# Optimization experiments

Measured on AMD Instinct MI355X. Metric: run time of the kernel, lower is better.

The kernel has to match this reference:

```python
import jax, jax.numpy as jnp
import numpy as np

IN_FEATURES = 4096
OUT_FEATURES = 4096
OUTLIER_NUM = 128
Q_IN = IN_FEATURES - OUTLIER_NUM  # 3968
B, S = 4, 2048


def _build_perm(seed=0):
    rng = np.random.default_rng(seed)
    outlier_ids = rng.choice(IN_FEATURES, size=OUTLIER_NUM, replace=False)
    mask = np.ones(IN_FEATURES, dtype=bool)
    mask[outlier_ids] = False
    col_ids = np.arange(IN_FEATURES, dtype=np.int32)
    col_perm = np.concatenate([col_ids[mask], col_ids[~mask]])
    inv_col_perm = np.zeros(IN_FEATURES, dtype=np.int32)
    inv_col_perm[col_perm] = np.arange(IN_FEATURES, dtype=np.int32)
    return inv_col_perm


def setup_inputs() -> dict:
    key = jax.random.key(0)
    k1, k2, k3, k4, k5 = jax.random.split(key, 5)
    inp = {
        "input": jax.random.normal(k1, (B, S, IN_FEATURES), dtype=jnp.float32),
        # low-bit integer codes stored as float (e.g. int4 range), per-row scale
        "q_weight": jax.random.randint(k2, (OUT_FEATURES, Q_IN), -8, 8).astype(jnp.float32),
        "fp_weight": jax.random.normal(k3, (OUT_FEATURES, OUTLIER_NUM), dtype=jnp.float32),
        "alpha_scale": jax.random.uniform(k4, (OUT_FEATURES, 1), dtype=jnp.float32, minval=0.01, maxval=0.1),
        "bias": jax.random.normal(k5, (OUT_FEATURES,), dtype=jnp.float32),
        "inv_col_perm": jnp.asarray(_build_perm(), dtype=jnp.int32),
    }
    return inp


def reference(input, q_weight, fp_weight, alpha_scale, bias, inv_col_perm):
    # SymQuant.dequantize: per-output-row symmetric scale
    dq_w = q_weight * alpha_scale                      # [O, Q_IN]
    out_w = jnp.concatenate([dq_w, fp_weight], axis=1)  # [O, IN]
    out_w = out_w[:, inv_col_perm]                      # undo column permutation
    # F.linear: input @ out_w.T + bias
    return jnp.einsum("bsi,oi->bso", input, out_w) + bias
```

## Files before the change

### kernel.cpp

```cpp
#include <hip/hip_runtime.h>
#include <stdint.h>

#define IN_F  4096
#define OUT_F 4096
#define OUTL  128
#define QIN   (IN_F - OUTL)
#define MTOT  8192
#define BM 128
#define BN 128
#define BKB 128

typedef unsigned short u16;
typedef int i32x4 __attribute__((ext_vector_type(4)));

__global__ __launch_bounds__(256) void prep_fused(
    const float* __restrict__ A, signed char* __restrict__ A8,
    float* __restrict__ s_arr,
    const float* __restrict__ qw, const float* __restrict__ fpw,
    const float* __restrict__ alpha, const int* __restrict__ invp,
    signed char* __restrict__ W8, float* __restrict__ t_arr) {
  const int tid = threadIdx.x;
  __shared__ float red[4];

  if (blockIdx.x >= OUT_F) {
    const int m = blockIdx.x - OUT_F;
    const float* row = A + (size_t)m * IN_F;
    float4 v[4];
    float amax = 0.f;
#pragma unroll
    for (int k = 0; k < 4; ++k) {
      v[k] = ((const float4*)row)[k * 256 + tid];
      amax = fmaxf(amax, fmaxf(fmaxf(fabsf(v[k].x), fabsf(v[k].y)),
                               fmaxf(fabsf(v[k].z), fabsf(v[k].w))));
    }
#pragma unroll
    for (int off = 32; off; off >>= 1)
      amax = fmaxf(amax, __shfl_xor(amax, off, 64));
    if ((tid & 63) == 0) red[tid >> 6] = amax;
    __syncthreads();
    amax = fmaxf(fmaxf(red[0], red[1]), fmaxf(red[2], red[3]));
    const float inv = 127.f / amax;
    if (tid == 0) s_arr[m] = amax / 127.f;
#pragma unroll
    for (int k = 0; k < 4; ++k) {
      const int q0 = __float2int_rn(v[k].x * inv);
      const int q1 = __float2int_rn(v[k].y * inv);
      const int q2 = __float2int_rn(v[k].z * inv);
      const int q3 = __float2int_rn(v[k].w * inv);
      const uint32_t p = (q0 & 255) | ((q1 & 255) << 8) |
                         ((q2 & 255) << 16) | ((uint32_t)(q3 & 255) << 24);
      ((uint32_t*)A8)[(size_t)m * (IN_F / 4) + k * 256 + tid] = p;
    }
  } else {
    const int o = blockIdx.x;
    __shared__ float qs[QIN];
    __shared__ float fs[OUTL];
    const float a = alpha[o];
    float amax = 0.f;
    const float4* qrow = (const float4*)(qw + (size_t)o * QIN);
#pragma unroll
    for (int k = 0; k < 4; ++k) {
      const int idx = k * 256 + tid;
      if (idx < QIN / 4) {
        const float4 q = qrow[idx];
        ((float4*)qs)[idx] = q;
        const float qm = fmaxf(fmaxf(fabsf(q.x), fabsf(q.y)),
                               fmaxf(fabsf(q.z), fabsf(q.w)));
        amax = fmaxf(amax, qm * a);
      }
    }
    if (tid < OUTL / 4) {
      const float4 f = ((const float4*)(fpw + (size_t)o * OUTL))[tid];
      ((float4*)fs)[tid] = f;
      amax = fmaxf(amax, fmaxf(fmaxf(fabsf(f.x), fabsf(f.y)),
                               fmaxf(fabsf(f.z), fabsf(f.w))));
    }
#pragma unroll
    for (int off = 32; off; off >>= 1)
      amax = fmaxf(amax, __shfl_xor(amax, off, 64));
    if ((tid & 63) == 0) red[tid >> 6] = amax;
    __syncthreads();
    amax = fmaxf(fmaxf(red[0], red[1]), fmaxf(red[2], red[3]));
    const float invws = 127.f / amax;
    if (tid == 0) t_arr[o] = amax / 127.f;

    signed char vals[16];
#pragma unroll
    for (int q = 0; q < 4; ++q) {
      const int4 jj = ((const int4*)invp)[tid * 4 + q];
      const int j[4] = {jj.x, jj.y, jj.z, jj.w};
#pragma unroll
      for (int e = 0; e < 4; ++e) {
        const float v = (j[e] < QIN) ? qs[j[e]] * a : fs[j[e] - QIN];
        vals[q * 4 + e] = (signed char)__float2int_rn(v * invws);
      }
    }
    ((uint4*)(W8 + (size_t)o * IN_F))[tid] = *(const uint4*)vals;
  }
}

#define GLDS(g, l)                                                              \
  __builtin_amdgcn_global_load_lds(                                             \
      (const __attribute__((address_space(1))) void*)(g),                       \
      (__attribute__((address_space(3))) void*)(l), 16, 0, 0)

__global__ __launch_bounds__(256, 3) void gemm_i8(
    const signed char* __restrict__ A8, const signed char* __restrict__ W8,
    const float* __restrict__ s_arr, const float* __restrict__ t_arr,
    const float* __restrict__ bias, float* __restrict__ C) {
  __shared__ unsigned char As8[BM * BKB];
  __shared__ unsigned char Bs8[BN * BKB];

  const int tid  = threadIdx.x;
  const int wave = tid >> 6;
  const int lane = tid & 63;
  const int bn = blockIdx.x, bm = blockIdx.y;
  const int wm = (wave >> 1) * 64;
  const int wn = (wave & 1)  * 64;

  const int srow   = wave * 32 + (lane >> 3);
  const int schunk = (lane & 7) ^ ((lane >> 3) & 7);
  const signed char* Ag = A8 + (size_t)(bm * BM + srow) * IN_F + schunk * 16;
  const signed char* Wg = W8 + (size_t)(bn * BN + srow) * IN_F + schunk * 16;
  unsigned char* AsW = As8 + wave * 32 * BKB;
  unsigned char* BsW = Bs8 + wave * 32 * BKB;

  i32x4 acc[4][4];
#pragma unroll
  for (int mi = 0; mi < 4; ++mi)
#pragma unroll
    for (int ni = 0; ni < 4; ++ni) acc[mi][ni] = (i32x4){0, 0, 0, 0};

  const int fr = lane & 15;
  const int fq = lane >> 4;

  for (int kt = 0; kt < IN_F / BKB; ++kt) {
    __syncthreads();
#pragma unroll
    for (int t = 0; t < 4; ++t) {
      GLDS(Ag + kt * BKB + t * 8 * IN_F, AsW + t * 8 * BKB);
      GLDS(Wg + kt * BKB + t * 8 * IN_F, BsW + t * 8 * BKB);
    }
    __syncthreads();

#pragma unroll
    for (int ks = 0; ks < 2; ++ks) {
      i32x4 af[4], bg[4];
#pragma unroll
      for (int mi = 0; mi < 4; ++mi)
        af[mi] = *(const i32x4*)
            &As8[(wm + mi * 16 + fr) * BKB + (((ks * 4 + fq) ^ (fr & 7)) * 16)];
#pragma unroll
      for (int ni = 0; ni < 4; ++ni)
        bg[ni] = *(const i32x4*)
            &Bs8[(wn + ni * 16 + fr) * BKB + (((ks * 4 + fq) ^ (fr & 7)) * 16)];
#pragma unroll
      for (int mi = 0; mi < 4; ++mi)
#pragma unroll
        for (int ni = 0; ni < 4; ++ni)
          acc[mi][ni] = __builtin_amdgcn_mfma_i32_16x16x64_i8(
              af[mi], bg[ni], acc[mi][ni], 0, 0, 0);
    }
  }

  float sv[4][4];
#pragma unroll
  for (int mi = 0; mi < 4; ++mi)
#pragma unroll
    for (int rr = 0; rr < 4; ++rr)
      sv[mi][rr] = s_arr[bm * BM + wm + mi * 16 + fq * 4 + rr];

#pragma unroll
  for (int ni = 0; ni < 4; ++ni) {
    const int n = bn * BN + wn + ni * 16 + fr;
    const float tn = t_arr[n];
    const float bv = bias[n];
#pragma unroll
    for (int mi = 0; mi < 4; ++mi) {
      const int m0 = bm * BM + wm + mi * 16 + fq * 4;
#pragma unroll
      for (int rr = 0; rr < 4; ++rr)
        C[(size_t)(m0 + rr) * OUT_F + n] =
            (float)acc[mi][ni][rr] * (sv[mi][rr] * tn) + bv;
    }
  }
}

extern "C" void kernel_launch(void* const* d_in, const int* in_sizes, int n_in,
                              void* d_out, int out_size, void* d_ws, size_t ws_size,
                              hipStream_t stream) {
  const float* input = (const float*)d_in[0];
  const float* qw    = (const float*)d_in[1];
  const float* fpw   = (const float*)d_in[2];
  const float* alpha = (const float*)d_in[3];
  const float* bias  = (const float*)d_in[4];
  const int*   invp  = (const int*)d_in[5];

  char* ws = (char*)d_ws;
  signed char* A8    = (signed char*)ws;
  signed char* W8    = (signed char*)(ws + (32ull << 20));
  float* s_arr = (float*)(ws + (48ull << 20));
  float* t_arr = (float*)(ws + (48ull << 20) + (64ull << 10));
  float* out = (float*)d_out;

  prep_fused<<<OUT_F + MTOT, 256, 0, stream>>>(input, A8, s_arr, qw, fpw,
                                               alpha, invp, W8, t_arr);

  dim3 ggrid(OUT_F / BN, MTOT / BM);
  gemm_i8<<<ggrid, dim3(256), 0, stream>>>(A8, W8, s_arr, t_arr, bias, out);
}
```

Measured before the change: 409.9 us.

## Double-buffer int8 GEMM with 256x256 tiles, 512 threads and swizzled block order

Grows the GEMM tile from 128x128 to 256x256 with 8 waves, each holding a 128x64 accumulator. K tiles are double-buffered so the next tile's global-to-LDS loads overlap the current tile's MFMAs, and a remapped 1D grid groups blocks for better cache locality. MFMA sections get raised wave priority. The prep kernel also pads its shared staging array to reduce LDS bank conflicts in the permuted gather. The cost is higher register and LDS pressure and only 512 blocks in the grid.

```diff
diff --git a/kernel.cpp b/kernel.cpp
--- a/kernel.cpp
+++ b/kernel.cpp
@@ -6,9 +6,10 @@
 #define OUTL  128
 #define QIN   (IN_F - OUTL)
 #define MTOT  8192
-#define BM 128
-#define BN 128
+#define BM 256
+#define BN 256
 #define BKB 128
+#define NKT (IN_F / BKB)
 
 typedef unsigned short u16;
 typedef int i32x4 __attribute__((ext_vector_type(4)));
@@ -53,7 +54,7 @@
     }
   } else {
     const int o = blockIdx.x;
-    __shared__ float qs[QIN];
+    __shared__ float qs[QIN + (QIN >> 4)];
     __shared__ float fs[OUTL];
     const float a = alpha[o];
     float amax = 0.f;
@@ -63,7 +64,11 @@
       const int idx = k * 256 + tid;
       if (idx < QIN / 4) {
         const float4 q = qrow[idx];
-        ((float4*)qs)[idx] = q;
+        const int b0 = idx * 4 + (idx >> 2);
+        qs[b0]     = q.x;
+        qs[b0 + 1] = q.y;
+        qs[b0 + 2] = q.z;
+        qs[b0 + 3] = q.w;
         const float qm = fmaxf(fmaxf(fabsf(q.x), fabsf(q.y)),
                                fmaxf(fabsf(q.z), fabsf(q.w)));
         amax = fmaxf(amax, qm * a);
@@ -91,7 +96,8 @@
       const int j[4] = {jj.x, jj.y, jj.z, jj.w};
 #pragma unroll
       for (int e = 0; e < 4; ++e) {
-        const float v = (j[e] < QIN) ? qs[j[e]] * a : fs[j[e] - QIN];
+        const int je = j[e];
+        const float v = (je < QIN) ? qs[je + (je >> 4)] * a : fs[je - QIN];
         vals[q * 4 + e] = (signed char)__float2int_rn(v * invws);
       }
     }
@@ -104,68 +110,93 @@
       (const __attribute__((address_space(1))) void*)(g),                       \
       (__attribute__((address_space(3))) void*)(l), 16, 0, 0)
 
-__global__ __launch_bounds__(256, 3) void gemm_i8(
+__global__ __launch_bounds__(512, 2) void gemm_i8(
     const signed char* __restrict__ A8, const signed char* __restrict__ W8,
     const float* __restrict__ s_arr, const float* __restrict__ t_arr,
     const float* __restrict__ bias, float* __restrict__ C) {
-  __shared__ unsigned char As8[BM * BKB];
-  __shared__ unsigned char Bs8[BN * BKB];
+  __shared__ unsigned char As8[2][BM * BKB];
+  __shared__ unsigned char Bs8[2][BN * BKB];
 
   const int tid  = threadIdx.x;
   const int wave = tid >> 6;
   const int lane = tid & 63;
-  const int bn = blockIdx.x, bm = blockIdx.y;
-  const int wm = (wave >> 1) * 64;
-  const int wn = (wave & 1)  * 64;
+
+  const int bid = ((blockIdx.x & 7) << 6) | ((int)blockIdx.x >> 3);
+  const int bm = bid >> 4;
+  const int bn = bid & 15;
+
+  const int wm = (wave >> 2) * 128;
+  const int wn = (wave & 3) * 64;
 
   const int srow   = wave * 32 + (lane >> 3);
   const int schunk = (lane & 7) ^ ((lane >> 3) & 7);
   const signed char* Ag = A8 + (size_t)(bm * BM + srow) * IN_F + schunk * 16;
   const signed char* Wg = W8 + (size_t)(bn * BN + srow) * IN_F + schunk * 16;
-  unsigned char* AsW = As8 + wave * 32 * BKB;
-  unsigned char* BsW = Bs8 + wave * 32 * BKB;
-
-  i32x4 acc[4][4];
-#pragma unroll
-  for (int mi = 0; mi < 4; ++mi)
+  const int sdst = wave * 32 * BKB;
+
+  i32x4 acc[8][4];
+#pragma unroll
+  for (int mi = 0; mi < 8; ++mi)
 #pragma unroll
     for (int ni = 0; ni < 4; ++ni) acc[mi][ni] = (i32x4){0, 0, 0, 0};
 
   const int fr = lane & 15;
   const int fq = lane >> 4;
 
-  for (int kt = 0; kt < IN_F / BKB; ++kt) {
-    __syncthreads();
+  int aoff[8], boff[4], ck[2];
+  ck[0] = ((0 + fq) ^ (fr & 7)) * 16;
+  ck[1] = ((4 + fq) ^ (fr & 7)) * 16;
+#pragma unroll
+  for (int mi = 0; mi < 8; ++mi) aoff[mi] = (wm + mi * 16 + fr) * BKB;
+#pragma unroll
+  for (int ni = 0; ni < 4; ++ni) boff[ni] = (wn + ni * 16 + fr) * BKB;
+
+  auto STAGE = [&](int buf, int kt) {
 #pragma unroll
     for (int t = 0; t < 4; ++t) {
-      GLDS(Ag + kt * BKB + t * 8 * IN_F, AsW + t * 8 * BKB);
-      GLDS(Wg + kt * BKB + t * 8 * IN_F, BsW + t * 8 * BKB);
-    }
-    __syncthreads();
-
+      GLDS(Ag + (size_t)kt * BKB + t * 8 * IN_F, &As8[buf][sdst + t * 8 * BKB]);
+      GLDS(Wg + (size_t)kt * BKB + t * 8 * IN_F, &Bs8[buf][sdst + t * 8 * BKB]);
+    }
+  };
+
+  auto COMPUTE = [&](int buf) {
 #pragma unroll
     for (int ks = 0; ks < 2; ++ks) {
-      i32x4 af[4], bg[4];
-#pragma unroll
-      for (int mi = 0; mi < 4; ++mi)
-        af[mi] = *(const i32x4*)
-            &As8[(wm + mi * 16 + fr) * BKB + (((ks * 4 + fq) ^ (fr & 7)) * 16)];
+      i32x4 bg[4], af[8];
 #pragma unroll
       for (int ni = 0; ni < 4; ++ni)
-        bg[ni] = *(const i32x4*)
-            &Bs8[(wn + ni * 16 + fr) * BKB + (((ks * 4 + fq) ^ (fr & 7)) * 16)];
-#pragma unroll
-      for (int mi = 0; mi < 4; ++mi)
+        bg[ni] = *(const i32x4*)&Bs8[buf][boff[ni] + ck[ks]];
+#pragma unroll
+      for (int mi = 0; mi < 8; ++mi)
+        af[mi] = *(const i32x4*)&As8[buf][aoff[mi] + ck[ks]];
+      __builtin_amdgcn_s_setprio(1);
+#pragma unroll
+      for (int mi = 0; mi < 8; ++mi)
 #pragma unroll
         for (int ni = 0; ni < 4; ++ni)
           acc[mi][ni] = __builtin_amdgcn_mfma_i32_16x16x64_i8(
               af[mi], bg[ni], acc[mi][ni], 0, 0, 0);
-    }
+      __builtin_amdgcn_s_setprio(0);
+    }
+  };
+
+  STAGE(0, 0);
+
+  for (int kt = 0; kt < NKT - 1; ++kt) {
+    STAGE((kt & 1) ^ 1, kt + 1);
+    asm volatile("s_waitcnt vmcnt(8)" ::: "memory");
+    __builtin_amdgcn_s_barrier();
+    COMPUTE(kt & 1);
+    asm volatile("s_waitcnt lgkmcnt(0)" ::: "memory");
+    __builtin_amdgcn_s_barrier();
   }
-
-  float sv[4][4];
-#pragma unroll
-  for (int mi = 0; mi < 4; ++mi)
+  asm volatile("s_waitcnt vmcnt(0)" ::: "memory");
+  __builtin_amdgcn_s_barrier();
+  COMPUTE((NKT - 1) & 1);
+
+  float sv[8][4];
+#pragma unroll
+  for (int mi = 0; mi < 8; ++mi)
 #pragma unroll
     for (int rr = 0; rr < 4; ++rr)
       sv[mi][rr] = s_arr[bm * BM + wm + mi * 16 + fq * 4 + rr];
@@ -176,7 +207,7 @@
     const float tn = t_arr[n];
     const float bv = bias[n];
 #pragma unroll
-    for (int mi = 0; mi < 4; ++mi) {
+    for (int mi = 0; mi < 8; ++mi) {
       const int m0 = bm * BM + wm + mi * 16 + fq * 4;
 #pragma unroll
       for (int rr = 0; rr < 4; ++rr)
@@ -206,6 +237,6 @@
   prep_fused<<<OUT_F + MTOT, 256, 0, stream>>>(input, A8, s_arr, qw, fpw,
                                                alpha, invp, W8, t_arr);
 
-  dim3 ggrid(OUT_F / BN, MTOT / BM);
-  gemm_i8<<<ggrid, dim3(256), 0, stream>>>(A8, W8, s_arr, t_arr, bias, out);
+  gemm_i8<<<dim3((MTOT / BM) * (OUT_F / BN)), dim3(512), 0, stream>>>(
+      A8, W8, s_arr, t_arr, bias, out);
 }
```

Result: no change. 413.7 us (+0.9%).

## Switch GEMM to 32x32x32 int8 MFMA, remap blocks, pad weight LDS

Applied to the files above, without the earlier changes.

The int8 GEMM's per-wave tiling moves from 16x16x64 MFMA to 32x32x32 MFMA, with four k-substeps per tile, precomputed LDS offsets and an epilogue rewritten for the 32x32 output layout. Fewer fragment loads per MFMA reduce LDS read traffic. The grid becomes 1D with a swizzled block-to-tile mapping, likely for XCD/L2 locality. The prep kernel pads its shared weight row to cut bank conflicts in the permuted gather and hoists the permutation loads ahead of the reduction barrier. The risks are higher accumulator register pressure at 3 blocks per CU and a less coalesced epilogue store pattern.

```diff
diff --git a/kernel.cpp b/kernel.cpp
--- a/kernel.cpp
+++ b/kernel.cpp
@@ -9,9 +9,11 @@
 #define BM 128
 #define BN 128
 #define BKB 128
+#define NKT (IN_F / BKB)
 
 typedef unsigned short u16;
-typedef int i32x4 __attribute__((ext_vector_type(4)));
+typedef int i32x4  __attribute__((ext_vector_type(4)));
+typedef int i32x16 __attribute__((ext_vector_type(16)));
 
 __global__ __launch_bounds__(256) void prep_fused(
     const float* __restrict__ A, signed char* __restrict__ A8,
@@ -53,7 +55,7 @@
     }
   } else {
     const int o = blockIdx.x;
-    __shared__ float qs[QIN];
+    __shared__ float qs[QIN + (QIN >> 4)];
     __shared__ float fs[OUTL];
     const float a = alpha[o];
     float amax = 0.f;
@@ -63,7 +65,11 @@
       const int idx = k * 256 + tid;
       if (idx < QIN / 4) {
         const float4 q = qrow[idx];
-        ((float4*)qs)[idx] = q;
+        const int b0 = idx * 4 + (idx >> 2);
+        qs[b0]     = q.x;
+        qs[b0 + 1] = q.y;
+        qs[b0 + 2] = q.z;
+        qs[b0 + 3] = q.w;
         const float qm = fmaxf(fmaxf(fabsf(q.x), fabsf(q.y)),
                                fmaxf(fabsf(q.z), fabsf(q.w)));
         amax = fmaxf(amax, qm * a);
@@ -75,6 +81,9 @@
       amax = fmaxf(amax, fmaxf(fmaxf(fabsf(f.x), fabsf(f.y)),
                                fmaxf(fabsf(f.z), fabsf(f.w))));
     }
+    int4 jj[4];
+#pragma unroll
+    for (int q = 0; q < 4; ++q) jj[q] = ((const int4*)invp)[tid * 4 + q];
 #pragma unroll
     for (int off = 32; off; off >>= 1)
       amax = fmaxf(amax, __shfl_xor(amax, off, 64));
@@ -87,11 +96,11 @@
     signed char vals[16];
 #pragma unroll
     for (int q = 0; q < 4; ++q) {
-      const int4 jj = ((const int4*)invp)[tid * 4 + q];
-      const int j[4] = {jj.x, jj.y, jj.z, jj.w};
+      const int j[4] = {jj[q].x, jj[q].y, jj[q].z, jj[q].w};
 #pragma unroll
       for (int e = 0; e < 4; ++e) {
-        const float v = (j[e] < QIN) ? qs[j[e]] * a : fs[j[e] - QIN];
+        const int je = j[e];
+        const float v = (je < QIN) ? qs[je + (je >> 4)] * a : fs[je - QIN];
         vals[q * 4 + e] = (signed char)__float2int_rn(v * invws);
       }
     }
@@ -114,7 +123,11 @@
   const int tid  = threadIdx.x;
   const int wave = tid >> 6;
   const int lane = tid & 63;
-  const int bn = blockIdx.x, bm = blockIdx.y;
+
+  const int bid = ((blockIdx.x & 7) << 8) | ((int)blockIdx.x >> 3);
+  const int bm = bid >> 5;
+  const int bn = bid & 31;
+
   const int wm = (wave >> 1) * 64;
   const int wn = (wave & 1)  * 64;
 
@@ -125,16 +138,26 @@
   unsigned char* AsW = As8 + wave * 32 * BKB;
   unsigned char* BsW = Bs8 + wave * 32 * BKB;
 
-  i32x4 acc[4][4];
-#pragma unroll
-  for (int mi = 0; mi < 4; ++mi)
-#pragma unroll
-    for (int ni = 0; ni < 4; ++ni) acc[mi][ni] = (i32x4){0, 0, 0, 0};
-
-  const int fr = lane & 15;
-  const int fq = lane >> 4;
-
-  for (int kt = 0; kt < IN_F / BKB; ++kt) {
+  i32x16 acc[2][2];
+#pragma unroll
+  for (int mi = 0; mi < 2; ++mi)
+#pragma unroll
+    for (int ni = 0; ni < 2; ++ni)
+#pragma unroll
+      for (int e = 0; e < 16; ++e) acc[mi][ni][e] = 0;
+
+  const int fr = lane & 31;
+  const int fh = lane >> 5;
+
+  int aoff[2], boff[2], ck[4];
+#pragma unroll
+  for (int mi = 0; mi < 2; ++mi) aoff[mi] = (wm + mi * 32 + fr) * BKB;
+#pragma unroll
+  for (int ni = 0; ni < 2; ++ni) boff[ni] = (wn + ni * 32 + fr) * BKB;
+#pragma unroll
+  for (int ks = 0; ks < 4; ++ks) ck[ks] = (((ks * 2 + fh) ^ (fr & 7)) * 16);
+
+  for (int kt = 0; kt < NKT; ++kt) {
     __syncthreads();
 #pragma unroll
     for (int t = 0; t < 4; ++t) {
@@ -144,44 +167,44 @@
     __syncthreads();
 
 #pragma unroll
-    for (int ks = 0; ks < 2; ++ks) {
-      i32x4 af[4], bg[4];
-#pragma unroll
-      for (int mi = 0; mi < 4; ++mi)
-        af[mi] = *(const i32x4*)
-            &As8[(wm + mi * 16 + fr) * BKB + (((ks * 4 + fq) ^ (fr & 7)) * 16)];
-#pragma unroll
-      for (int ni = 0; ni < 4; ++ni)
-        bg[ni] = *(const i32x4*)
-            &Bs8[(wn + ni * 16 + fr) * BKB + (((ks * 4 + fq) ^ (fr & 7)) * 16)];
-#pragma unroll
-      for (int mi = 0; mi < 4; ++mi)
-#pragma unroll
-        for (int ni = 0; ni < 4; ++ni)
-          acc[mi][ni] = __builtin_amdgcn_mfma_i32_16x16x64_i8(
+    for (int ks = 0; ks < 4; ++ks) {
+      i32x4 af[2], bg[2];
+#pragma unroll
+      for (int mi = 0; mi < 2; ++mi)
+        af[mi] = *(const i32x4*)&As8[aoff[mi] + ck[ks]];
+#pragma unroll
+      for (int ni = 0; ni < 2; ++ni)
+        bg[ni] = *(const i32x4*)&Bs8[boff[ni] + ck[ks]];
+#pragma unroll
+      for (int mi = 0; mi < 2; ++mi)
+#pragma unroll
+        for (int ni = 0; ni < 2; ++ni)
+          acc[mi][ni] = __builtin_amdgcn_mfma_i32_32x32x32_i8(
               af[mi], bg[ni], acc[mi][ni], 0, 0, 0);
     }
   }
 
-  float sv[4][4];
-#pragma unroll
-  for (int mi = 0; mi < 4; ++mi)
-#pragma unroll
-    for (int rr = 0; rr < 4; ++rr)
-      sv[mi][rr] = s_arr[bm * BM + wm + mi * 16 + fq * 4 + rr];
-
-#pragma unroll
-  for (int ni = 0; ni < 4; ++ni) {
-    const int n = bn * BN + wn + ni * 16 + fr;
+  float sv[2][16];
+#pragma unroll
+  for (int mi = 0; mi < 2; ++mi)
+#pragma unroll
+    for (int r = 0; r < 16; ++r)
+      sv[mi][r] =
+          s_arr[bm * BM + wm + mi * 32 + (r & 3) + 8 * (r >> 2) + 4 * fh];
+
+#pragma unroll
+  for (int ni = 0; ni < 2; ++ni) {
+    const int n = bn * BN + wn + ni * 32 + fr;
     const float tn = t_arr[n];
     const float bv = bias[n];
 #pragma unroll
-    for (int mi = 0; mi < 4; ++mi) {
-      const int m0 = bm * BM + wm + mi * 16 + fq * 4;
-#pragma unroll
-      for (int rr = 0; rr < 4; ++rr)
-        C[(size_t)(m0 + rr) * OUT_F + n] =
-            (float)acc[mi][ni][rr] * (sv[mi][rr] * tn) + bv;
+    for (int mi = 0; mi < 2; ++mi) {
+      const int m0 = bm * BM + wm + mi * 32 + 4 * fh;
+#pragma unroll
+      for (int r = 0; r < 16; ++r) {
+        const int m = m0 + (r & 3) + 8 * (r >> 2);
+        C[(size_t)m * OUT_F + n] = (float)acc[mi][ni][r] * (sv[mi][r] * tn) + bv;
+      }
     }
   }
 }
@@ -206,6 +229,6 @@
   prep_fused<<<OUT_F + MTOT, 256, 0, stream>>>(input, A8, s_arr, qw, fpw,
                                                alpha, invp, W8, t_arr);
 
-  dim3 ggrid(OUT_F / BN, MTOT / BM);
-  gemm_i8<<<ggrid, dim3(256), 0, stream>>>(A8, W8, s_arr, t_arr, bias, out);
+  gemm_i8<<<dim3((MTOT / BM) * (OUT_F / BN)), dim3(256), 0, stream>>>(
+      A8, W8, s_arr, t_arr, bias, out);
 }
```

Measured after the change: 427.8 us. +4.4%, slower.
